# Performance work log

Hardware: AMD Instinct MI355X
Metric: run time of the kernel (lower is better)

Reference implementation:

```python
import jax, jax.numpy as jnp
import numpy as np

HIDDEN = 128
LOCAL_HEADS = 4
GLOBAL_HEADS = 2
N_NODES = 10000
E_LOCAL = 320000
E_GLOBAL = 640000
NEG_SLOPE = 0.2  # PyG GATv2Conv default


def _glorot(key, shape):
    fan_in, fan_out = shape[0], shape[-1]
    s = jnp.sqrt(6.0 / (fan_in + fan_out))
    return jax.random.uniform(key, shape, jnp.float32, -s, s)


def setup_inputs() -> dict:
    key = jax.random.key(0)
    ks = jax.random.split(key, 16)
    H1, H2 = LOCAL_HEADS, GLOBAL_HEADS
    d = HIDDEN
    inp = {
        "x": jax.random.normal(ks[0], (N_NODES, d), jnp.float32),
        "edge_index": jax.random.randint(ks[1], (2, E_LOCAL), 0, N_NODES, jnp.int32),
        "global_edge_index": jax.random.randint(ks[2], (2, E_GLOBAL), 0, N_NODES, jnp.int32),
        # conv1 (local) params
        "Wl1": _glorot(ks[3], (d, H1 * d)),
        "bl1": jnp.zeros((H1 * d,), jnp.float32),
        "Wr1": _glorot(ks[4], (d, H1 * d)),
        "br1": jnp.zeros((H1 * d,), jnp.float32),
        "att1": _glorot(ks[5], (H1, d)),
        "b1": jnp.zeros((H1 * d,), jnp.float32),
        # conv2 (global) params
        "Wl2": _glorot(ks[6], (d, H2 * d)),
        "bl2": jnp.zeros((H2 * d,), jnp.float32),
        "Wr2": _glorot(ks[7], (d, H2 * d)),
        "br2": jnp.zeros((H2 * d,), jnp.float32),
        "att2": _glorot(ks[8], (H2, d)),
        "b2": jnp.zeros((H2 * d,), jnp.float32),
        # final fc: hidden*(H1+H2) -> hidden
        "Wfc": _glorot(ks[9], (d * (H1 + H2), d)),
        "bfc": jnp.zeros((d,), jnp.float32),
    }
    return inp


def gatv2_layer(x, edge, Wl, bl, Wr, br, att, bias, heads):
    # PyG GATv2Conv: concat=True, add_self_loops=True, share_weights=False
    N = x.shape[0]
    HC = Wl.shape[1]
    C = HC // heads
    loops = jnp.arange(N, dtype=edge.dtype)
    src = jnp.concatenate([edge[0], loops])  # message source j
    dst = jnp.concatenate([edge[1], loops])  # message target i
    xl = (x @ Wl + bl).reshape(N, heads, C)  # source transform
    xr = (x @ Wr + br).reshape(N, heads, C)  # target transform
    s = jax.nn.leaky_relu(xl[src] + xr[dst], NEG_SLOPE)        # [E,H,C]
    logits = jnp.einsum('ehc,hc->eh', s, att)                   # [E,H]
    m = jax.ops.segment_max(logits, dst, num_segments=N)       # segment softmax
    a = jnp.exp(logits - m[dst])
    denom = jax.ops.segment_sum(a, dst, num_segments=N)
    alpha = a / denom[dst]                                      # [E,H]
    out = jax.ops.segment_sum(alpha[:, :, None] * xl[src], dst, num_segments=N)
    return out.reshape(N, HC) + bias


def reference(x, edge_index, global_edge_index,
              Wl1, bl1, Wr1, br1, att1, b1,
              Wl2, bl2, Wr2, br2, att2, b2,
              Wfc, bfc):
    x1 = gatv2_layer(x, edge_index, Wl1, bl1, Wr1, br1, att1, b1, LOCAL_HEADS)
    x2 = gatv2_layer(x, global_edge_index, Wl2, bl2, Wr2, br2, att2, b2, GLOBAL_HEADS)
    h = jnp.concatenate([x1, x2], axis=-1)  # [N, hidden*(H1+H2)]
    return h @ Wfc + bfc                     # [N, hidden]
```

## Files before the change

### kernel.cpp

```cpp
#include <hip/hip_runtime.h>

#define N_NODES 10000
#define E_LOCAL 320000
#define E_GLOBAL 640000
#define CNT_LEN 10240
#define NB 160
#define BCAP1 3072
#define BCAP2 5632
#define CHUNK 2048
#define NWG_L 157
#define NWG_G 313

typedef __attribute__((ext_vector_type(8))) short short8;
typedef __attribute__((ext_vector_type(4))) float f32x4;
typedef __attribute__((ext_vector_type(4))) unsigned short ushort4v;
typedef __attribute__((ext_vector_type(2))) unsigned int uint2v;
typedef __attribute__((ext_vector_type(4))) unsigned int uint4v;

typedef __attribute__((address_space(1))) const void* gas_ptr;
typedef __attribute__((address_space(3))) void* lds_ptr;

__device__ __forceinline__ unsigned short f2bf(float f) {
  union { unsigned int i; float f; } v; v.f = f;
  unsigned int r = (v.i + 0x7FFF + ((v.i >> 16) & 1)) >> 16;
  return (unsigned short)r;
}
__device__ __forceinline__ void gld_lds16(const void* g, void* l) {
  __builtin_amdgcn_global_load_lds((gas_ptr)g, (lds_ptr)l, 16, 0, 0);
}

template<int NW> struct WVecT;
template<> struct WVecT<4> { using T = uint4v; };
template<> struct WVecT<2> { using T = uint2v; };

template<int NW, typename WV>
__device__ __forceinline__ void w2f(WV w, float* f) {
  #pragma unroll
  for (int i = 0; i < NW; ++i) {
    union { unsigned int u; float x; } lo, hi;
    lo.u = w[i] << 16; hi.u = w[i] & 0xffff0000u;
    f[2 * i] = lo.x; f[2 * i + 1] = hi.x;
  }
}

template<int CTRL>
__device__ __forceinline__ float dppadd(float v) {
  int s = __builtin_amdgcn_update_dpp(0, __float_as_int(v), CTRL, 0xf, 0xf, true);
  return v + __int_as_float(s);
}
__device__ __forceinline__ float red16(float v) {
  v = dppadd<0xB1>(v);
  v = dppadd<0x4E>(v);
  v = dppadd<0x140>(v);
  v = dppadd<0x141>(v);
  return v;
}

__global__ __launch_bounds__(256) void prep(
    const float* __restrict__ x,
    const float* __restrict__ Wl1, const float* __restrict__ Wr1,
    const float* __restrict__ Wl2, const float* __restrict__ Wr2,
    const float* __restrict__ Wfc,
    const float* __restrict__ bl1, const float* __restrict__ br1,
    const float* __restrict__ bl2, const float* __restrict__ br2,
    ushort* __restrict__ xb, ushort* __restrict__ wt_all,
    ushort* __restrict__ wtfc, float* __restrict__ bias_all,
    int* __restrict__ bcur) {
  __shared__ float tl[32][33];
  int b = blockIdx.x;
  const int tid = threadIdx.x;
  if (b < 1250) {
    int i = b * 256 + tid;
    if (i < 320000) {
      float4 f = reinterpret_cast<const float4*>(x)[i];
      ushort4v o; o[0] = f2bf(f.x); o[1] = f2bf(f.y); o[2] = f2bf(f.z); o[3] = f2bf(f.w);
      reinterpret_cast<ushort4v*>(xb)[i] = o;
    }
    return;
  }
  b -= 1250;
  if (b < 288) {
    const float* W; ushort* dst; int N, nOff, ldK; int t = b;
    if (t < 64)       { W = Wl1; dst = wt_all; N = 512; nOff = 0;    ldK = 128; }
    else if (t < 128) { W = Wr1; dst = wt_all; N = 512; nOff = 512;  ldK = 128; t -= 64; }
    else if (t < 160) { W = Wl2; dst = wt_all; N = 256; nOff = 1024; ldK = 128; t -= 128; }
    else if (t < 192) { W = Wr2; dst = wt_all; N = 256; nOff = 1280; ldK = 128; t -= 160; }
    else              { W = Wfc; dst = wtfc;   N = 128; nOff = 0;    ldK = 768; t -= 192; }
    const int ntn = N / 32;
    const int n0 = (t % ntn) * 32, k0 = (t / ntn) * 32;
    const int tx = tid & 31, ty = tid >> 5;
    #pragma unroll
    for (int j = 0; j < 4; ++j)
      tl[ty + j * 8][tx] = W[(size_t)(k0 + ty + j * 8) * N + n0 + tx];
    __syncthreads();
    #pragma unroll
    for (int j = 0; j < 4; ++j)
      dst[(size_t)(nOff + n0 + ty + j * 8) * ldK + k0 + tx] = f2bf(tl[tx][ty + j * 8]);
    return;
  }
  for (int i = tid; i < 1536; i += 256) {
    float v = i < 512 ? bl1[i] : i < 1024 ? br1[i - 512]
            : i < 1280 ? bl2[i - 1024] : br2[i - 1280];
    bias_all[i] = v;
  }
  for (int i = tid; i < 2 * NB; i += 256) bcur[i] = 0;
}

template<bool OUT_BF16, int K>
__global__ __launch_bounds__(256) void gemm_mfma(
    const ushort* __restrict__ A, const ushort* __restrict__ Bt,
    const float* __restrict__ bias, void* __restrict__ outv,
    int M, int N, int ldOut) {
  __shared__ ushort As[2][64 * 32];
  __shared__ ushort Bs[2][64 * 32];
  const int tid  = threadIdx.x;
  const int wave = tid >> 6;
  const int lane = tid & 63;
  const int row0 = blockIdx.y * 64;
  const int col0 = blockIdx.x * 64;
  const int srow = tid >> 2;
  const int schunk = tid & 3;
  int ar = row0 + srow; if (ar >= M) ar = M - 1;
  const ushort* aSrc = A  + (size_t)ar * K + schunk * 8;
  const ushort* bSrc = Bt + (size_t)(col0 + srow) * K + schunk * 8;
  const int ldsOff = tid * 8;
  const int fr = lane & 15;
  const int kc = lane >> 4;

  f32x4 c[4];
  #pragma unroll
  for (int f = 0; f < 4; ++f) { c[f][0] = 0.f; c[f][1] = 0.f; c[f][2] = 0.f; c[f][3] = 0.f; }

  constexpr int NK = K / 32;
  gld_lds16(aSrc, &As[0][ldsOff]);
  gld_lds16(bSrc, &Bs[0][ldsOff]);
  #pragma unroll
  for (int kk = 0; kk < NK; ++kk) {
    const int cur = kk & 1;
    __syncthreads();
    if (kk + 1 < NK) {
      gld_lds16(aSrc + (kk + 1) * 32, &As[cur ^ 1][ldsOff]);
      gld_lds16(bSrc + (kk + 1) * 32, &Bs[cur ^ 1][ldsOff]);
    }
    short8 a = *reinterpret_cast<const short8*>(&As[cur][(wave * 16 + fr) * 32 + kc * 8]);
    #pragma unroll
    for (int f = 0; f < 4; ++f) {
      short8 b = *reinterpret_cast<const short8*>(&Bs[cur][(f * 16 + fr) * 32 + kc * 8]);
      c[f] = __builtin_amdgcn_mfma_f32_16x16x32_bf16(a, b, c[f], 0, 0, 0);
    }
  }
  const int orow = row0 + wave * 16 + (lane >> 4) * 4;
  #pragma unroll
  for (int f = 0; f < 4; ++f) {
    const int col = col0 + f * 16 + fr;
    const float bv = bias ? bias[col] : 0.f;
    #pragma unroll
    for (int q = 0; q < 4; ++q) {
      const int r = orow + q;
      if (r < M) {
        float v = c[f][q] + bv;
        if (OUT_BF16) ((ushort*)outv)[(size_t)r * ldOut + col] = f2bf(v);
        else          ((float*) outv)[(size_t)r * ldOut + col] = v;
      }
    }
  }
}

__global__ __launch_bounds__(256) void bucketize(
    const int* __restrict__ sl, const int* __restrict__ dl,
    const int* __restrict__ sg, const int* __restrict__ dg,
    int* __restrict__ bcur, uint2* __restrict__ bb1, uint2* __restrict__ bb2) {
  __shared__ int h[NB];
  __shared__ int cur[NB];
  const int tid = threadIdx.x;
  int wg = blockIdx.x;
  const int* S; const int* D; int E0, Etot; uint2* BB; int* BC; int cap;
  if (wg < NWG_L) { S = sl; D = dl; E0 = wg * CHUNK; Etot = E_LOCAL;  BB = bb1; BC = bcur;      cap = BCAP1; }
  else { wg -= NWG_L; S = sg; D = dg; E0 = wg * CHUNK; Etot = E_GLOBAL; BB = bb2; BC = bcur + NB; cap = BCAP2; }
  for (int i = tid; i < NB; i += 256) h[i] = 0;
  __syncthreads();
  int myd[8], mys[8];
  #pragma unroll
  for (int k = 0; k < 8; ++k) {
    int e = E0 + k * 256 + tid;
    if (e < Etot) { myd[k] = D[e]; mys[k] = S[e]; atomicAdd(&h[myd[k] >> 6], 1); }
    else myd[k] = -1;
  }
  __syncthreads();
  for (int b = tid; b < NB; b += 256)
    cur[b] = h[b] ? atomicAdd(&BC[b], h[b]) : 0;
  __syncthreads();
  #pragma unroll
  for (int k = 0; k < 8; ++k) {
    if (myd[k] >= 0) {
      int b = myd[k] >> 6;
      int pos = atomicAdd(&cur[b], 1);
      if (pos < cap) BB[(size_t)b * cap + pos] = make_uint2((unsigned)mys[k], (unsigned)myd[k]);
    }
  }
}

__global__ __launch_bounds__(320) void scanb(const int* __restrict__ bcur,
                                             int* __restrict__ base) {
  __shared__ int v[2 * NB];
  __shared__ int sz[2 * NB];
  const int t = threadIdx.x;
  const int ls = (t < NB) ? 0 : NB;
  int s = min(bcur[t], (t < NB) ? BCAP1 : BCAP2);
  sz[t] = s; v[t] = s;
  __syncthreads();
  for (int o = 1; o < NB; o <<= 1) {
    int add = (t - o >= ls) ? v[t - o] : 0;
    __syncthreads();
    v[t] += add;
    __syncthreads();
  }
  base[t] = v[t] - sz[t];
}

__global__ __launch_bounds__(256) void csrbuild(
    const int* __restrict__ bcur, const int* __restrict__ base,
    const uint2* __restrict__ bb1, const uint2* __restrict__ bb2,
    int* __restrict__ csr1, int* __restrict__ csr2,
    int* __restrict__ off1, int* __restrict__ off2) {
  __shared__ int nh[64];
  __shared__ int ncur[64];
  const int tid = threadIdx.x;
  const int b = blockIdx.x;
  const uint2* BB; int* csr; int* off; int cap; int bi;
  if (b < NB) { BB = bb1; csr = csr1; off = off1; cap = BCAP1; bi = b; }
  else        { BB = bb2; csr = csr2; off = off2; cap = BCAP2; bi = b - NB; }
  const int n = min(bcur[b], cap);
  const uint2* P = BB + (size_t)bi * cap;
  if (tid < 64) nh[tid] = 0;
  __syncthreads();
  for (int i = tid; i < n; i += 256) atomicAdd(&nh[P[i].y & 63], 1);
  __syncthreads();
  if (tid == 0) {
    int s = base[b];
    #pragma unroll 4
    for (int j = 0; j < 64; ++j) { int c = nh[j]; nh[j] = s; s += c; }
  }
  __syncthreads();
  if (tid < 64) { off[bi * 64 + tid] = nh[tid]; ncur[tid] = nh[tid]; }
  __syncthreads();
  for (int i = tid; i < n; i += 256) {
    uint2 p = P[i];
    int pos = atomicAdd(&ncur[p.y & 63], 1);
    csr[pos] = (int)p.x;
  }
}

template<int H, int U>
__device__ __forceinline__ void agg_block(
    const ushort* __restrict__ xl, const ushort* __restrict__ xr,
    const float* __restrict__ att, const int* __restrict__ csr,
    const int* __restrict__ off, const float* __restrict__ bias,
    int inLd, ushort* __restrict__ outp, int outLd, int node,
    float* __restrict__ sacc, float* __restrict__ sden) {
  constexpr int TC = H * 128;
  constexpr int PER = TC / 64;
  constexpr int NW = PER / 2;
  constexpr int GRP = 64 / H;
  using WVec = typename WVecT<NW>::T;
  const int tid = threadIdx.x;
  const int wave = tid >> 6;
  const int lane = tid & 63;
  const int base = lane * PER;
  const int head = lane / GRP;

  float attv[PER], xri[PER], acc[PER];
  #pragma unroll
  for (int p = 0; p < PER; ++p) attv[p] = att[base + p] * 1.4426950408889634f;
  {
    WVec r = *reinterpret_cast<const WVec*>(&xr[(size_t)node * inLd + base]);
    w2f<NW>(r, xri);
  }
  #pragma unroll
  for (int p = 0; p < PER; ++p) acc[p] = 0.f;
  float den = 0.f;

  const int e0n = off[node], e1n = off[node + 1];
  const int chunk = (e1n - e0n + 3) >> 2;
  const int e0 = e0n + wave * chunk;
  const int e1 = min(e0 + chunk, e1n);

  if (wave == 0) {
    WVec r = *reinterpret_cast<const WVec*>(&xl[(size_t)node * inLd + base]);
    float xs[PER]; w2f<NW>(r, xs);
    float d = 0.f;
    #pragma unroll
    for (int p = 0; p < PER; ++p) {
      float t = xs[p] + xri[p];
      t = fmaxf(t, 0.2f * t);
      d = fmaf(t, attv[p], d);
    }
    d = red16(d);
    if (GRP == 32) d += __shfl_xor(d, 16, 64);
    float wgt = exp2f(d);
    den = wgt;
    #pragma unroll
    for (int p = 0; p < PER; ++p) acc[p] = wgt * xs[p];
  }

  auto loadIdx = [&](int bb, int* ii) {
    #pragma unroll
    for (int m = 0; m < U; ++m) ii[m] = csr[e0 + bb * U + m];
  };
  auto loadRows = [&](const int* ii, WVec* rr) {
    #pragma unroll
    for (int m = 0; m < U; ++m)
      rr[m] = *reinterpret_cast<const WVec*>(&xl[(size_t)ii[m] * inLd + base]);
  };
  auto computeB = [&](WVec* rr) {
    float pp[U]; float xs[U][PER];
    #pragma unroll
    for (int m = 0; m < U; ++m) {
      w2f<NW>(rr[m], xs[m]);
      float d = 0.f;
      #pragma unroll
      for (int p = 0; p < PER; ++p) {
        float t = xs[m][p] + xri[p];
        t = fmaxf(t, 0.2f * t);
        d = fmaf(t, attv[p], d);
      }
      pp[m] = d;
    }
    #pragma unroll
    for (int m = 0; m < U; ++m) pp[m] = red16(pp[m]);
    if (GRP == 32) {
      #pragma unroll
      for (int m = 0; m < U; ++m) pp[m] += __shfl_xor(pp[m], 16, 64);
    }
    #pragma unroll
    for (int m = 0; m < U; ++m) {
      float wgt = exp2f(pp[m]);
      den += wgt;
      #pragma unroll
      for (int p = 0; p < PER; ++p) acc[p] = fmaf(wgt, xs[m][p], acc[p]);
    }
  };

  const int nb = (e1 - e0) / U;
  WVec rA[U], rB[U];
  int iA[U], iB[U];
  if (nb > 0) { loadIdx(0, iA); loadRows(iA, rA); }
  if (nb > 1) loadIdx(1, iB);
  int b = 0;
  for (; b + 2 <= nb; b += 2) {
    loadRows(iB, rB);
    if (b + 2 < nb) loadIdx(b + 2, iA);
    computeB(rA);
    if (b + 2 < nb) loadRows(iA, rA);
    if (b + 3 < nb) loadIdx(b + 3, iB);
    computeB(rB);
  }
  if (b < nb) computeB(rA);
  for (int e = e0 + nb * U; e < e1; ++e) {
    int s = csr[e];
    WVec r = *reinterpret_cast<const WVec*>(&xl[(size_t)s * inLd + base]);
    float xs[PER]; w2f<NW>(r, xs);
    float d = 0.f;
    #pragma unroll
    for (int p = 0; p < PER; ++p) {
      float t = xs[p] + xri[p];
      t = fmaxf(t, 0.2f * t);
      d = fmaf(t, attv[p], d);
    }
    d = red16(d);
    if (GRP == 32) d += __shfl_xor(d, 16, 64);
    float wgt = exp2f(d);
    den += wgt;
    #pragma unroll
    for (int p = 0; p < PER; ++p) acc[p] = fmaf(wgt, xs[p], acc[p]);
  }

  #pragma unroll
  for (int p = 0; p < PER; ++p) sacc[wave * TC + base + p] = acc[p];
  if ((lane & (GRP - 1)) == 0) sden[wave * H + head] = den;
  __syncthreads();
  constexpr int CH = TC / 256;
  #pragma unroll
  for (int j = 0; j < CH; ++j) {
    const int c = tid * CH + j;
    float s = sacc[c] + sacc[TC + c] + sacc[2 * TC + c] + sacc[3 * TC + c];
    const int h = c >> 7;
    float dt = sden[h] + sden[H + h] + sden[2 * H + h] + sden[3 * H + h];
    outp[(size_t)node * outLd + c] = f2bf(s / dt + bias[c]);
  }
}

__global__ __launch_bounds__(256) void aggregate2(
    const ushort* __restrict__ feat,
    const float* __restrict__ att1, const float* __restrict__ att2,
    const int* __restrict__ csr1, const int* __restrict__ off1,
    const float* __restrict__ b1,
    const int* __restrict__ csr2, const int* __restrict__ off2,
    const float* __restrict__ b2,
    ushort* __restrict__ hb) {
  __shared__ float sacc[4 * 512];
  __shared__ float sden[16];
  const int nd = blockIdx.x;
  if (nd < N_NODES)
    agg_block<4, 3>(feat, feat + 512, att1, csr1, off1, b1, 1536, hb, 768,
                    nd, sacc, sden);
  else
    agg_block<2, 4>(feat + 1024, feat + 1280, att2, csr2, off2, b2, 1536,
                    hb + 512, 768, nd - N_NODES, sacc, sden);
}

extern "C" void kernel_launch(void* const* d_in, const int* in_sizes, int n_in,
                              void* d_out, int out_size, void* d_ws, size_t ws_size,
                              hipStream_t stream) {
  const float* x    = (const float*)d_in[0];
  const int*   ei   = (const int*)d_in[1];
  const int*   gei  = (const int*)d_in[2];
  const float* Wl1  = (const float*)d_in[3];
  const float* bl1  = (const float*)d_in[4];
  const float* Wr1  = (const float*)d_in[5];
  const float* br1  = (const float*)d_in[6];
  const float* att1 = (const float*)d_in[7];
  const float* b1   = (const float*)d_in[8];
  const float* Wl2  = (const float*)d_in[9];
  const float* bl2  = (const float*)d_in[10];
  const float* Wr2  = (const float*)d_in[11];
  const float* br2  = (const float*)d_in[12];
  const float* att2 = (const float*)d_in[13];
  const float* b2   = (const float*)d_in[14];
  const float* Wfc  = (const float*)d_in[15];
  const float* bfc  = (const float*)d_in[16];
  float* out = (float*)d_out;

  char* w = (char*)d_ws;
  ushort* xb     = (ushort*)w; w += (size_t)N_NODES * 128 * 2;
  ushort* feat   = (ushort*)w; w += (size_t)N_NODES * 1536 * 2;
  ushort* hb     = (ushort*)w; w += (size_t)N_NODES * 768 * 2;
  ushort* wt_all = (ushort*)w; w += (size_t)1536 * 128 * 2;
  ushort* wtfc   = (ushort*)w; w += (size_t)128 * 768 * 2;
  float* bias_all = (float*)w; w += 1536 * 4;
  int* off1 = (int*)w;            w += (size_t)CNT_LEN * 4;
  int* off2 = (int*)w;            w += (size_t)CNT_LEN * 4;
  int* csr1 = (int*)w;            w += (size_t)E_LOCAL * 4;
  int* csr2 = (int*)w;            w += (size_t)E_GLOBAL * 4;
  int* bcur = (int*)w;            w += 2 * NB * 4;
  int* bbase = (int*)w;           w += 2 * NB * 4;
  uint2* bb1 = (uint2*)w;         w += (size_t)NB * BCAP1 * 8;
  uint2* bb2 = (uint2*)w;         w += (size_t)NB * BCAP2 * 8;

  const int N = N_NODES;
  prep<<<1539, 256, 0, stream>>>(x, Wl1, Wr1, Wl2, Wr2, Wfc,
                                 bl1, br1, bl2, br2,
                                 xb, wt_all, wtfc, bias_all, bcur);

  bucketize<<<NWG_L + NWG_G, 256, 0, stream>>>(
      ei, ei + E_LOCAL, gei, gei + E_GLOBAL, bcur, bb1, bb2);
  scanb<<<1, 320, 0, stream>>>(bcur, bbase);
  csrbuild<<<2 * NB, 256, 0, stream>>>(bcur, bbase, bb1, bb2,
                                       csr1, csr2, off1, off2);

  gemm_mfma<true, 128><<<dim3(24, 157), 256, 0, stream>>>(
      xb, wt_all, bias_all, feat, N, 1536, 1536);

  aggregate2<<<2 * N, 256, 0, stream>>>(feat, att1, att2,
                                        csr1, off1, b1, csr2, off2, b2, hb);

  gemm_mfma<false, 768><<<dim3(2, 157), 256, 0, stream>>>(hb, wtfc, bfc, out, N, 128, 128);
}
```

Before: 254.5 us.

## Fuse prep/bucketize and csrbuild/GEMM launches, drop scan via atomic segment offsets

Folds the seven-kernel pipeline into four launches. Prep and bucketize now run in one grid, and CSR build and the feature GEMM share another. The separate scan kernel is replaced by per-bucket atomic allocation of CSR segments, which needs separate start and end arrays because bucket order is no longer contiguous. The aggregation kernel stages the target row in LDS, makes neighbour indices wave-uniform with readfirstlane, and uses packed float2 arithmetic. The intent is to cut launch gaps and scalarize the gather addressing, at the cost of non-deterministic CSR ordering and an added memset.

```diff
diff --git a/kernel.cpp b/kernel.cpp
--- a/kernel.cpp
+++ b/kernel.cpp
@@ -3,16 +3,17 @@
 #define N_NODES 10000
 #define E_LOCAL 320000
 #define E_GLOBAL 640000
-#define CNT_LEN 10240
 #define NB 160
 #define BCAP1 3072
 #define BCAP2 5632
 #define CHUNK 2048
 #define NWG_L 157
 #define NWG_G 313
+#define L2E 1.4426950408889634f
 
 typedef __attribute__((ext_vector_type(8))) short short8;
 typedef __attribute__((ext_vector_type(4))) float f32x4;
+typedef __attribute__((ext_vector_type(2))) float float2v;
 typedef __attribute__((ext_vector_type(4))) unsigned short ushort4v;
 typedef __attribute__((ext_vector_type(2))) unsigned int uint2v;
 typedef __attribute__((ext_vector_type(4))) unsigned int uint4v;
@@ -28,20 +29,15 @@
 __device__ __forceinline__ void gld_lds16(const void* g, void* l) {
   __builtin_amdgcn_global_load_lds((gas_ptr)g, (lds_ptr)l, 16, 0, 0);
 }
+__device__ __forceinline__ float2v bf2x2(unsigned int w) {
+  union { unsigned int u[2]; float2v f; } v;
+  v.u[0] = w << 16; v.u[1] = w & 0xffff0000u;
+  return v.f;
+}
 
 template<int NW> struct WVecT;
 template<> struct WVecT<4> { using T = uint4v; };
 template<> struct WVecT<2> { using T = uint2v; };
-
-template<int NW, typename WV>
-__device__ __forceinline__ void w2f(WV w, float* f) {
-  #pragma unroll
-  for (int i = 0; i < NW; ++i) {
-    union { unsigned int u; float x; } lo, hi;
-    lo.u = w[i] << 16; hi.u = w[i] & 0xffff0000u;
-    f[2 * i] = lo.x; f[2 * i + 1] = hi.x;
-  }
-}
 
 template<int CTRL>
 __device__ __forceinline__ float dppadd(float v) {
@@ -56,18 +52,43 @@
   return v;
 }
 
-__global__ __launch_bounds__(256) void prep(
-    const float* __restrict__ x,
-    const float* __restrict__ Wl1, const float* __restrict__ Wr1,
-    const float* __restrict__ Wl2, const float* __restrict__ Wr2,
-    const float* __restrict__ Wfc,
-    const float* __restrict__ bl1, const float* __restrict__ br1,
-    const float* __restrict__ bl2, const float* __restrict__ br2,
-    ushort* __restrict__ xb, ushort* __restrict__ wt_all,
-    ushort* __restrict__ wtfc, float* __restrict__ bias_all,
-    int* __restrict__ bcur) {
+__device__ void bucketize_body(int wg, const int* sl, const int* dl,
+    const int* sg, const int* dg, int* bcur, uint2* bb1, uint2* bb2) {
+  __shared__ int h[NB];
+  __shared__ int cur[NB];
+  const int tid = threadIdx.x;
+  const int* S; const int* D; int E0, Etot; uint2* BB; int* BC; int cap;
+  if (wg < NWG_L) { S = sl; D = dl; E0 = wg * CHUNK; Etot = E_LOCAL;  BB = bb1; BC = bcur;      cap = BCAP1; }
+  else { wg -= NWG_L; S = sg; D = dg; E0 = wg * CHUNK; Etot = E_GLOBAL; BB = bb2; BC = bcur + NB; cap = BCAP2; }
+  for (int i = tid; i < NB; i += 256) h[i] = 0;
+  __syncthreads();
+  int myd[8], mys[8];
+  #pragma unroll
+  for (int k = 0; k < 8; ++k) {
+    int e = E0 + k * 256 + tid;
+    if (e < Etot) { myd[k] = D[e]; mys[k] = S[e]; atomicAdd(&h[myd[k] >> 6], 1); }
+    else myd[k] = -1;
+  }
+  __syncthreads();
+  for (int b = tid; b < NB; b += 256)
+    cur[b] = h[b] ? atomicAdd(&BC[b], h[b]) : 0;
+  __syncthreads();
+  #pragma unroll
+  for (int k = 0; k < 8; ++k) {
+    if (myd[k] >= 0) {
+      int b = myd[k] >> 6;
+      int pos = atomicAdd(&cur[b], 1);
+      if (pos < cap) BB[(size_t)b * cap + pos] = make_uint2((unsigned)mys[k], (unsigned)myd[k]);
+    }
+  }
+}
+
+__device__ void prep_body(int b,
+    const float* x, const float* Wl1, const float* Wr1,
+    const float* Wl2, const float* Wr2, const float* Wfc,
+    const float* bl1, const float* br1, const float* bl2, const float* br2,
+    ushort* xb, ushort* wt_all, ushort* wtfc, float* bias_all) {
   __shared__ float tl[32][33];
-  int b = blockIdx.x;
   const int tid = threadIdx.x;
   if (b < 1250) {
     int i = b * 256 + tid;
@@ -103,11 +124,63 @@
             : i < 1280 ? bl2[i - 1024] : br2[i - 1280];
     bias_all[i] = v;
   }
-  for (int i = tid; i < 2 * NB; i += 256) bcur[i] = 0;
+}
+
+__global__ __launch_bounds__(256) void k1_prep_bucket(
+    const int* ei, const int* gei,
+    const float* x, const float* Wl1, const float* Wr1,
+    const float* Wl2, const float* Wr2, const float* Wfc,
+    const float* bl1, const float* br1, const float* bl2, const float* br2,
+    ushort* xb, ushort* wt_all, ushort* wtfc, float* bias_all,
+    int* bcur, uint2* bb1, uint2* bb2) {
+  const int b = blockIdx.x;
+  if (b < NWG_L + NWG_G)
+    bucketize_body(b, ei, ei + E_LOCAL, gei, gei + E_GLOBAL, bcur, bb1, bb2);
+  else
+    prep_body(b - (NWG_L + NWG_G), x, Wl1, Wr1, Wl2, Wr2, Wfc,
+              bl1, br1, bl2, br2, xb, wt_all, wtfc, bias_all);
+}
+
+__device__ void csrbuild_body(int b, const int* bcur, int* gcur,
+    const uint2* bb1, const uint2* bb2,
+    int* csr1, int* csr2, int* st1, int* en1, int* st2, int* en2) {
+  __shared__ int nh[64];
+  __shared__ int ncur[64];
+  __shared__ int sbase;
+  const int tid = threadIdx.x;
+  const uint2* BB; int* csr; int* st; int* en; int cap; int bi; int layer;
+  if (b < NB) { BB = bb1; csr = csr1; st = st1; en = en1; cap = BCAP1; bi = b; layer = 0; }
+  else        { BB = bb2; csr = csr2; st = st2; en = en2; cap = BCAP2; bi = b - NB; layer = 1; }
+  const int n = min(bcur[b], cap);
+  if (tid == 0) sbase = atomicAdd(&gcur[layer], n);
+  if (tid < 64) nh[tid] = 0;
+  __syncthreads();
+  const uint2* P = BB + (size_t)bi * cap;
+  for (int i = tid; i < n; i += 256) atomicAdd(&nh[P[i].y & 63], 1);
+  __syncthreads();
+  int cnt = (tid < 64) ? nh[tid] : 0;
+  __syncthreads();
+  if (tid == 0) {
+    int s = sbase;
+    #pragma unroll 4
+    for (int j = 0; j < 64; ++j) { int c = nh[j]; nh[j] = s; s += c; }
+  }
+  __syncthreads();
+  if (tid < 64) {
+    st[bi * 64 + tid] = nh[tid];
+    en[bi * 64 + tid] = nh[tid] + cnt;
+    ncur[tid] = nh[tid];
+  }
+  __syncthreads();
+  for (int i = tid; i < n; i += 256) {
+    uint2 p = P[i];
+    int pos = atomicAdd(&ncur[p.y & 63], 1);
+    csr[pos] = (int)p.x;
+  }
 }
 
 template<bool OUT_BF16, int K>
-__global__ __launch_bounds__(256) void gemm_mfma(
+__device__ void gemm_body(int bx, int by,
     const ushort* __restrict__ A, const ushort* __restrict__ Bt,
     const float* __restrict__ bias, void* __restrict__ outv,
     int M, int N, int ldOut) {
@@ -116,8 +189,8 @@
   const int tid  = threadIdx.x;
   const int wave = tid >> 6;
   const int lane = tid & 63;
-  const int row0 = blockIdx.y * 64;
-  const int col0 = blockIdx.x * 64;
+  const int row0 = by * 64;
+  const int col0 = bx * 64;
   const int srow = tid >> 2;
   const int schunk = tid & 3;
   int ar = row0 + srow; if (ar >= M) ar = M - 1;
@@ -166,98 +239,36 @@
   }
 }
 
-__global__ __launch_bounds__(256) void bucketize(
-    const int* __restrict__ sl, const int* __restrict__ dl,
-    const int* __restrict__ sg, const int* __restrict__ dg,
-    int* __restrict__ bcur, uint2* __restrict__ bb1, uint2* __restrict__ bb2) {
-  __shared__ int h[NB];
-  __shared__ int cur[NB];
-  const int tid = threadIdx.x;
-  int wg = blockIdx.x;
-  const int* S; const int* D; int E0, Etot; uint2* BB; int* BC; int cap;
-  if (wg < NWG_L) { S = sl; D = dl; E0 = wg * CHUNK; Etot = E_LOCAL;  BB = bb1; BC = bcur;      cap = BCAP1; }
-  else { wg -= NWG_L; S = sg; D = dg; E0 = wg * CHUNK; Etot = E_GLOBAL; BB = bb2; BC = bcur + NB; cap = BCAP2; }
-  for (int i = tid; i < NB; i += 256) h[i] = 0;
-  __syncthreads();
-  int myd[8], mys[8];
-  #pragma unroll
-  for (int k = 0; k < 8; ++k) {
-    int e = E0 + k * 256 + tid;
-    if (e < Etot) { myd[k] = D[e]; mys[k] = S[e]; atomicAdd(&h[myd[k] >> 6], 1); }
-    else myd[k] = -1;
-  }
-  __syncthreads();
-  for (int b = tid; b < NB; b += 256)
-    cur[b] = h[b] ? atomicAdd(&BC[b], h[b]) : 0;
-  __syncthreads();
-  #pragma unroll
-  for (int k = 0; k < 8; ++k) {
-    if (myd[k] >= 0) {
-      int b = myd[k] >> 6;
-      int pos = atomicAdd(&cur[b], 1);
-      if (pos < cap) BB[(size_t)b * cap + pos] = make_uint2((unsigned)mys[k], (unsigned)myd[k]);
-    }
-  }
-}
-
-__global__ __launch_bounds__(320) void scanb(const int* __restrict__ bcur,
-                                             int* __restrict__ base) {
-  __shared__ int v[2 * NB];
-  __shared__ int sz[2 * NB];
-  const int t = threadIdx.x;
-  const int ls = (t < NB) ? 0 : NB;
-  int s = min(bcur[t], (t < NB) ? BCAP1 : BCAP2);
-  sz[t] = s; v[t] = s;
-  __syncthreads();
-  for (int o = 1; o < NB; o <<= 1) {
-    int add = (t - o >= ls) ? v[t - o] : 0;
-    __syncthreads();
-    v[t] += add;
-    __syncthreads();
-  }
-  base[t] = v[t] - sz[t];
-}
-
-__global__ __launch_bounds__(256) void csrbuild(
-    const int* __restrict__ bcur, const int* __restrict__ base,
-    const uint2* __restrict__ bb1, const uint2* __restrict__ bb2,
-    int* __restrict__ csr1, int* __restrict__ csr2,
-    int* __restrict__ off1, int* __restrict__ off2) {
-  __shared__ int nh[64];
-  __shared__ int ncur[64];
-  const int tid = threadIdx.x;
+__global__ __launch_bounds__(256) void k2_csr_gemm(
+    const int* bcur, int* gcur, const uint2* bb1, const uint2* bb2,
+    int* csr1, int* csr2, int* st1, int* en1, int* st2, int* en2,
+    const ushort* xb, const ushort* wt_all, const float* bias_all,
+    ushort* feat) {
   const int b = blockIdx.x;
-  const uint2* BB; int* csr; int* off; int cap; int bi;
-  if (b < NB) { BB = bb1; csr = csr1; off = off1; cap = BCAP1; bi = b; }
-  else        { BB = bb2; csr = csr2; off = off2; cap = BCAP2; bi = b - NB; }
-  const int n = min(bcur[b], cap);
-  const uint2* P = BB + (size_t)bi * cap;
-  if (tid < 64) nh[tid] = 0;
-  __syncthreads();
-  for (int i = tid; i < n; i += 256) atomicAdd(&nh[P[i].y & 63], 1);
-  __syncthreads();
-  if (tid == 0) {
-    int s = base[b];
-    #pragma unroll 4
-    for (int j = 0; j < 64; ++j) { int c = nh[j]; nh[j] = s; s += c; }
-  }
-  __syncthreads();
-  if (tid < 64) { off[bi * 64 + tid] = nh[tid]; ncur[tid] = nh[tid]; }
-  __syncthreads();
-  for (int i = tid; i < n; i += 256) {
-    uint2 p = P[i];
-    int pos = atomicAdd(&ncur[p.y & 63], 1);
-    csr[pos] = (int)p.x;
-  }
+  if (b < 2 * NB) {
+    csrbuild_body(b, bcur, gcur, bb1, bb2, csr1, csr2, st1, en1, st2, en2);
+    return;
+  }
+  const int g = b - 2 * NB;
+  gemm_body<true, 128>(g % 24, g / 24, xb, wt_all, bias_all, feat,
+                       N_NODES, 1536, 1536);
+}
+
+__global__ __launch_bounds__(256) void k4_fc(
+    const ushort* hb, const ushort* wtfc, const float* bfc, float* out) {
+  gemm_body<false, 768>(blockIdx.x & 1, blockIdx.x >> 1, hb, wtfc, bfc, out,
+                        N_NODES, 128, 128);
 }
 
 template<int H, int U>
 __device__ __forceinline__ void agg_block(
     const ushort* __restrict__ xl, const ushort* __restrict__ xr,
     const float* __restrict__ att, const int* __restrict__ csr,
-    const int* __restrict__ off, const float* __restrict__ bias,
-    int inLd, ushort* __restrict__ outp, int outLd, int node,
-    float* __restrict__ sacc, float* __restrict__ sden) {
+    const int* __restrict__ st, const int* __restrict__ en,
+    const float* __restrict__ bias, int inLd,
+    ushort* __restrict__ outp, int outLd, int node,
+    float* __restrict__ sacc, float* __restrict__ sden,
+    ushort* __restrict__ srow) {
   constexpr int TC = H * 128;
   constexpr int PER = TC / 64;
   constexpr int NW = PER / 2;
@@ -269,38 +280,47 @@
   const int base = lane * PER;
   const int head = lane / GRP;
 
-  float attv[PER], xri[PER], acc[PER];
-  #pragma unroll
-  for (int p = 0; p < PER; ++p) attv[p] = att[base + p] * 1.4426950408889634f;
   {
-    WVec r = *reinterpret_cast<const WVec*>(&xr[(size_t)node * inLd + base]);
-    w2f<NW>(r, xri);
-  }
-  #pragma unroll
-  for (int p = 0; p < PER; ++p) acc[p] = 0.f;
+    const ushort* xrrow = xr + (size_t)node * inLd;
+    for (int i = tid; i < TC / 8; i += 256)
+      *reinterpret_cast<short8*>(srow + i * 8) =
+          *reinterpret_cast<const short8*>(xrrow + i * 8);
+  }
+  __syncthreads();
+
+  float2v attv[NW], xri[NW], acc[NW];
+  #pragma unroll
+  for (int w = 0; w < NW; ++w) {
+    attv[w][0] = att[base + 2 * w] * L2E;
+    attv[w][1] = att[base + 2 * w + 1] * L2E;
+    xri[w] = bf2x2(*reinterpret_cast<const unsigned int*>(srow + base + 2 * w));
+    acc[w][0] = 0.f; acc[w][1] = 0.f;
+  }
   float den = 0.f;
 
-  const int e0n = off[node], e1n = off[node + 1];
+  const int e0n = st[node], e1n = en[node];
   const int chunk = (e1n - e0n + 3) >> 2;
   const int e0 = e0n + wave * chunk;
   const int e1 = min(e0 + chunk, e1n);
 
   if (wave == 0) {
-    WVec r = *reinterpret_cast<const WVec*>(&xl[(size_t)node * inLd + base]);
-    float xs[PER]; w2f<NW>(r, xs);
-    float d = 0.f;
-    #pragma unroll
-    for (int p = 0; p < PER; ++p) {
-      float t = xs[p] + xri[p];
-      t = fmaxf(t, 0.2f * t);
-      d = fmaf(t, attv[p], d);
-    }
-    d = red16(d);
+    const WVec r = *reinterpret_cast<const WVec*>(xl + (size_t)node * inLd + base);
+    float2v d2 = {0.f, 0.f};
+    float2v xs[NW];
+    #pragma unroll
+    for (int w = 0; w < NW; ++w) {
+      xs[w] = bf2x2(r[w]);
+      float2v t2 = xs[w] + xri[w];
+      t2 = __builtin_elementwise_max(t2, t2 * 0.2f);
+      d2 = __builtin_elementwise_fma(t2, attv[w], d2);
+    }
+    float d = red16(d2[0] + d2[1]);
     if (GRP == 32) d += __shfl_xor(d, 16, 64);
     float wgt = exp2f(d);
     den = wgt;
-    #pragma unroll
-    for (int p = 0; p < PER; ++p) acc[p] = wgt * xs[p];
+    float2v w2 = {wgt, wgt};
+    #pragma unroll
+    for (int w = 0; w < NW; ++w) acc[w] = __builtin_elementwise_fma(w2, xs[w], acc[w]);
   }
 
   auto loadIdx = [&](int bb, int* ii) {
@@ -309,22 +329,25 @@
   };
   auto loadRows = [&](const int* ii, WVec* rr) {
     #pragma unroll
-    for (int m = 0; m < U; ++m)
-      rr[m] = *reinterpret_cast<const WVec*>(&xl[(size_t)ii[m] * inLd + base]);
+    for (int m = 0; m < U; ++m) {
+      const int sv = __builtin_amdgcn_readfirstlane(ii[m]);
+      rr[m] = *reinterpret_cast<const WVec*>(xl + (size_t)sv * inLd + base);
+    }
   };
   auto computeB = [&](WVec* rr) {
-    float pp[U]; float xs[U][PER];
+    float2v xs[U][NW];
+    float pp[U];
     #pragma unroll
     for (int m = 0; m < U; ++m) {
-      w2f<NW>(rr[m], xs[m]);
-      float d = 0.f;
+      float2v d2 = {0.f, 0.f};
       #pragma unroll
-      for (int p = 0; p < PER; ++p) {
-        float t = xs[m][p] + xri[p];
-        t = fmaxf(t, 0.2f * t);
-        d = fmaf(t, attv[p], d);
+      for (int w = 0; w < NW; ++w) {
+        xs[m][w] = bf2x2(rr[m][w]);
+        float2v t2 = xs[m][w] + xri[w];
+        t2 = __builtin_elementwise_max(t2, t2 * 0.2f);
+        d2 = __builtin_elementwise_fma(t2, attv[w], d2);
       }
-      pp[m] = d;
+      pp[m] = d2[0] + d2[1];
     }
     #pragma unroll
     for (int m = 0; m < U; ++m) pp[m] = red16(pp[m]);
@@ -336,8 +359,9 @@
     for (int m = 0; m < U; ++m) {
       float wgt = exp2f(pp[m]);
       den += wgt;
+      float2v w2 = {wgt, wgt};
       #pragma unroll
-      for (int p = 0; p < PER; ++p) acc[p] = fmaf(wgt, xs[m][p], acc[p]);
+      for (int w = 0; w < NW; ++w) acc[w] = __builtin_elementwise_fma(w2, xs[m][w], acc[w]);
     }
   };
 
@@ -357,26 +381,31 @@
   }
   if (b < nb) computeB(rA);
   for (int e = e0 + nb * U; e < e1; ++e) {
-    int s = csr[e];
-    WVec r = *reinterpret_cast<const WVec*>(&xl[(size_t)s * inLd + base]);
-    float xs[PER]; w2f<NW>(r, xs);
-    float d = 0.f;
-    #pragma unroll
-    for (int p = 0; p < PER; ++p) {
-      float t = xs[p] + xri[p];
-      t = fmaxf(t, 0.2f * t);
-      d = fmaf(t, attv[p], d);
-    }
-    d = red16(d);
+    const int sv = __builtin_amdgcn_readfirstlane(csr[e]);
+    const WVec r = *reinterpret_cast<const WVec*>(xl + (size_t)sv * inLd + base);
+    float2v d2 = {0.f, 0.f};
+    float2v xs[NW];
+    #pragma unroll
+    for (int w = 0; w < NW; ++w) {
+      xs[w] = bf2x2(r[w]);
+      float2v t2 = xs[w] + xri[w];
+      t2 = __builtin_elementwise_max(t2, t2 * 0.2f);
+      d2 = __builtin_elementwise_fma(t2, attv[w], d2);
+    }
+    float d = red16(d2[0] + d2[1]);
     if (GRP == 32) d += __shfl_xor(d, 16, 64);
     float wgt = exp2f(d);
     den += wgt;
-    #pragma unroll
-    for (int p = 0; p < PER; ++p) acc[p] = fmaf(wgt, xs[p], acc[p]);
-  }
-
-  #pragma unroll
-  for (int p = 0; p < PER; ++p) sacc[wave * TC + base + p] = acc[p];
+    float2v w2 = {wgt, wgt};
+    #pragma unroll
+    for (int w = 0; w < NW; ++w) acc[w] = __builtin_elementwise_fma(w2, xs[w], acc[w]);
+  }
+
+  #pragma unroll
+  for (int w = 0; w < NW; ++w) {
+    sacc[wave * TC + base + 2 * w]     = acc[w][0];
+    sacc[wave * TC + base + 2 * w + 1] = acc[w][1];
+  }
   if ((lane & (GRP - 1)) == 0) sden[wave * H + head] = den;
   __syncthreads();
   constexpr int CH = TC / 256;
@@ -393,20 +422,21 @@
 __global__ __launch_bounds__(256) void aggregate2(
     const ushort* __restrict__ feat,
     const float* __restrict__ att1, const float* __restrict__ att2,
-    const int* __restrict__ csr1, const int* __restrict__ off1,
-    const float* __restrict__ b1,
-    const int* __restrict__ csr2, const int* __restrict__ off2,
-    const float* __restrict__ b2,
+    const int* __restrict__ csr1, const int* __restrict__ st1,
+    const int* __restrict__ en1, const float* __restrict__ b1,
+    const int* __restrict__ csr2, const int* __restrict__ st2,
+    const int* __restrict__ en2, const float* __restrict__ b2,
     ushort* __restrict__ hb) {
   __shared__ float sacc[4 * 512];
   __shared__ float sden[16];
+  __shared__ ushort srow[512];
   const int nd = blockIdx.x;
   if (nd < N_NODES)
-    agg_block<4, 3>(feat, feat + 512, att1, csr1, off1, b1, 1536, hb, 768,
-                    nd, sacc, sden);
+    agg_block<4, 3>(feat, feat + 512, att1, csr1, st1, en1, b1, 1536, hb, 768,
+                    nd, sacc, sden, srow);
   else
-    agg_block<2, 4>(feat + 1024, feat + 1280, att2, csr2, off2, b2, 1536,
-                    hb + 512, 768, nd - N_NODES, sacc, sden);
+    agg_block<2, 4>(feat + 1024, feat + 1280, att2, csr2, st2, en2, b2, 1536,
+                    hb + 512, 768, nd - N_NODES, sacc, sden, srow);
 }
 
 extern "C" void kernel_launch(void* const* d_in, const int* in_sizes, int n_in,
@@ -438,31 +468,29 @@
   ushort* wt_all = (ushort*)w; w += (size_t)1536 * 128 * 2;
   ushort* wtfc   = (ushort*)w; w += (size_t)128 * 768 * 2;
   float* bias_all = (float*)w; w += 1536 * 4;
-  int* off1 = (int*)w;            w += (size_t)CNT_LEN * 4;
-  int* off2 = (int*)w;            w += (size_t)CNT_LEN * 4;
+  int* st1 = (int*)w;             w += (size_t)10240 * 4;
+  int* en1 = (int*)w;             w += (size_t)10240 * 4;
+  int* st2 = (int*)w;             w += (size_t)10240 * 4;
+  int* en2 = (int*)w;             w += (size_t)10240 * 4;
   int* csr1 = (int*)w;            w += (size_t)E_LOCAL * 4;
   int* csr2 = (int*)w;            w += (size_t)E_GLOBAL * 4;
   int* bcur = (int*)w;            w += 2 * NB * 4;
-  int* bbase = (int*)w;           w += 2 * NB * 4;
+  int* gcur = (int*)w;            w += 2 * 4;
   uint2* bb1 = (uint2*)w;         w += (size_t)NB * BCAP1 * 8;
   uint2* bb2 = (uint2*)w;         w += (size_t)NB * BCAP2 * 8;
 
-  const int N = N_NODES;
-  prep<<<1539, 256, 0, stream>>>(x, Wl1, Wr1, Wl2, Wr2, Wfc,
-                                 bl1, br1, bl2, br2,
-                                 xb, wt_all, wtfc, bias_all, bcur);
-
-  bucketize<<<NWG_L + NWG_G, 256, 0, stream>>>(
-      ei, ei + E_LOCAL, gei, gei + E_GLOBAL, bcur, bb1, bb2);
-  scanb<<<1, 320, 0, stream>>>(bcur, bbase);
-  csrbuild<<<2 * NB, 256, 0, stream>>>(bcur, bbase, bb1, bb2,
-                                       csr1, csr2, off1, off2);
-
-  gemm_mfma<true, 128><<<dim3(24, 157), 256, 0, stream>>>(
-      xb, wt_all, bias_all, feat, N, 1536, 1536);
-
-  aggregate2<<<2 * N, 256, 0, stream>>>(feat, att1, att2,
-                                        csr1, off1, b1, csr2, off2, b2, hb);
-
-  gemm_mfma<false, 768><<<dim3(2, 157), 256, 0, stream>>>(hb, wtfc, bfc, out, N, 128, 128);
-}
+  hipMemsetAsync(bcur, 0, (2 * NB + 2) * sizeof(int), stream);
+
+  k1_prep_bucket<<<NWG_L + NWG_G + 1539, 256, 0, stream>>>(
+      ei, gei, x, Wl1, Wr1, Wl2, Wr2, Wfc, bl1, br1, bl2, br2,
+      xb, wt_all, wtfc, bias_all, bcur, bb1, bb2);
+
+  k2_csr_gemm<<<2 * NB + 24 * 157, 256, 0, stream>>>(
+      bcur, gcur, bb1, bb2, csr1, csr2, st1, en1, st2, en2,
+      xb, wt_all, bias_all, feat);
+
+  aggregate2<<<2 * N_NODES, 256, 0, stream>>>(
+      feat, att1, att2, csr1, st1, en1, b1, csr2, st2, en2, b2, hb);
+
+  k4_fc<<<2 * 157, 256, 0, stream>>>(hb, wtfc, bfc, out);
+}
```

Result: no change. 252.2 us (-0.9%).
